# Kernel tuning notes

Measured on AMD Instinct MI355X. Metric: run time of the kernel, lower is better.

Reference implementation:

```python
import jax, jax.numpy as jnp
import numpy as np


def setup_inputs() -> dict:
    key = jax.random.key(0)
    ks = jax.random.split(key, 5)
    B, C, H, W = 8, 256, 64, 64
    Cr = 32  # in_channels // reduction_ratio
    s_in = 1.0 / np.sqrt(C)
    x = jax.random.normal(ks[0], (B, C, H, W), dtype=jnp.float32)
    Wq = jax.random.normal(ks[1], (Cr, C), dtype=jnp.float32) * s_in
    Wk = jax.random.normal(ks[2], (Cr, C), dtype=jnp.float32) * s_in
    Wv = jax.random.normal(ks[3], (C, C), dtype=jnp.float32) * s_in
    bq = jnp.zeros((Cr,), dtype=jnp.float32)
    bk = jnp.zeros((Cr,), dtype=jnp.float32)
    bv = jnp.zeros((C,), dtype=jnp.float32)
    gamma = jnp.ones((1,), dtype=jnp.float32)
    return {"x": x, "Wq": Wq, "bq": bq, "Wk": Wk, "bk": bk, "Wv": Wv, "bv": bv, "gamma": gamma}


def reference(x, Wq, bq, Wk, bk, Wv, bv, gamma):
    B, C, H, W = x.shape
    N = H * W
    xf = x.reshape(B, C, N)  # 1x1 conv == per-pixel linear over channels
    q = jnp.einsum('oc,bcn->bon', Wq, xf) + bq[None, :, None]   # [B, Cr, N]
    k = jnp.einsum('oc,bcn->bon', Wk, xf) + bk[None, :, None]   # [B, Cr, N]
    v = jnp.einsum('oc,bcn->bon', Wv, xf) + bv[None, :, None]   # [B, C, N]
    # correlations[b, i, j] = sum_c q[b, c, i] * k[b, c, j]
    corr = jnp.einsum('bci,bcj->bij', q, k)                     # [B, N, N]
    # NOTE: softmax over dim=1 (the i / query axis), as in the original torch code
    beta = jax.nn.softmax(corr, axis=1)
    att = gamma[0] * jnp.einsum('bci,bij->bcj', v, beta)        # [B, C, N]
    return att.reshape(B, C, H, W) + x
```

## Files before the change

### kernel.cpp

```cpp
#include <hip/hip_runtime.h>
#include <hip/hip_bf16.h>

typedef short bf16x8 __attribute__((ext_vector_type(8)));
typedef float f32x4 __attribute__((ext_vector_type(4)));
typedef unsigned short u16;

#define LOG2E 1.44269504088896340736f
#define AS1 __attribute__((address_space(1)))
#define AS3 __attribute__((address_space(3)))

__device__ __forceinline__ u16 f2bf(float f) {
    unsigned u = __float_as_uint(f);
    u += 0x7fffu + ((u >> 16) & 1u);
    return (u16)(u >> 16);
}
__device__ __forceinline__ float bf2f(u16 h) {
    return __uint_as_float(((unsigned)h) << 16);
}
__device__ __forceinline__ void gload_lds16(const void* g, void* l) {
    __builtin_amdgcn_global_load_lds((const AS1 unsigned int*)g,
                                     (AS3 unsigned int*)l, 16, 0, 0);
}

__global__ void k_prep(const float* __restrict__ Wq, const float* __restrict__ bq,
                       const float* __restrict__ Wk, const float* __restrict__ bk,
                       const float* __restrict__ Wv, const float* __restrict__ bv,
                       u16* __restrict__ Whi, u16* __restrict__ Wlo,
                       float* __restrict__ bias) {
    int idx = blockIdx.x * 256 + threadIdx.x;
    if (idx >= 320 * 256) return;
    int row = idx >> 8, c = idx & 255;
    float w, b;
    if (row < 256)      { w = Wv[row * 256 + c];                  b = bv[row]; }
    else if (row < 288) { w = Wq[(row - 256) * 256 + c] * LOG2E;  b = bq[row - 256] * LOG2E; }
    else                { w = Wk[(row - 288) * 256 + c];          b = bk[row - 288]; }
    u16 hi = f2bf(w);
    Whi[idx] = hi;
    Wlo[idx] = f2bf(w - bf2f(hi));
    if (c == 0) bias[row] = b;
}

#define XPAD 264

__global__ __launch_bounds__(256) void k_proj(
    const float* __restrict__ x, const u16* __restrict__ Whi,
    const u16* __restrict__ Wlo, const float* __restrict__ bias,
    u16* __restrict__ qt, u16* __restrict__ kt, u16* __restrict__ vbf) {
    __shared__ __attribute__((aligned(16))) u16 xh[64 * XPAD];
    __shared__ __attribute__((aligned(16))) u16 xl[64 * XPAD];
    int bid = blockIdx.x;
    int b = bid & 7, nt = bid >> 3;
    int n0 = nt * 64;
    int t = threadIdx.x;
    int lane = t & 63, w = t >> 6;
    int lr = lane & 15, lk = lane >> 4;

    {
        int n = t & 63;
        int cg = t >> 6;
        for (int it = 0; it < 8; ++it) {
            int c8 = (it * 4 + cg) * 8;
            bf16x8 hv, lv;
#pragma unroll
            for (int u = 0; u < 8; ++u) {
                float xv = x[((size_t)(b * 256 + c8 + u)) * 4096 + n0 + n];
                u16 hu = f2bf(xv);
                hv[u] = (short)hu;
                lv[u] = (short)f2bf(xv - bf2f(hu));
            }
            *(bf16x8*)&xh[n * XPAD + c8] = hv;
            *(bf16x8*)&xl[n * XPAD + c8] = lv;
        }
    }
    __syncthreads();

    f32x4 acc[5][4];
#pragma unroll
    for (int i = 0; i < 5; i++)
#pragma unroll
        for (int j = 0; j < 4; j++) acc[i][j] = (f32x4){0.f, 0.f, 0.f, 0.f};

    for (int cs = 0; cs < 8; ++cs) {
        int c0 = cs * 32;
        bf16x8 ah[5], al[5], bh[4], bl[4];
#pragma unroll
        for (int mt = 0; mt < 5; ++mt) {
            int row = (w * 5 + mt) * 16 + lr;
            ah[mt] = *(const bf16x8*)&Whi[row * 256 + c0 + lk * 8];
            al[mt] = *(const bf16x8*)&Wlo[row * 256 + c0 + lk * 8];
        }
#pragma unroll
        for (int ns = 0; ns < 4; ++ns) {
            int np = ns * 16 + lr;
            bh[ns] = *(const bf16x8*)&xh[np * XPAD + c0 + lk * 8];
            bl[ns] = *(const bf16x8*)&xl[np * XPAD + c0 + lk * 8];
        }
#pragma unroll
        for (int mt = 0; mt < 5; ++mt)
#pragma unroll
            for (int ns = 0; ns < 4; ++ns) {
                acc[mt][ns] = __builtin_amdgcn_mfma_f32_16x16x32_bf16(ah[mt], bh[ns], acc[mt][ns], 0, 0, 0);
                acc[mt][ns] = __builtin_amdgcn_mfma_f32_16x16x32_bf16(ah[mt], bl[ns], acc[mt][ns], 0, 0, 0);
                acc[mt][ns] = __builtin_amdgcn_mfma_f32_16x16x32_bf16(al[mt], bh[ns], acc[mt][ns], 0, 0, 0);
            }
    }

#pragma unroll
    for (int mt = 0; mt < 5; ++mt) {
        int tile = w * 5 + mt;
#pragma unroll
        for (int ns = 0; ns < 4; ++ns) {
#pragma unroll
            for (int r = 0; r < 4; ++r) {
                int row = tile * 16 + lk * 4 + r;
                int n = n0 + ns * 16 + lr;
                float val = acc[mt][ns][r] + bias[row];
                if (row < 256) {
                    vbf[((size_t)(b * 256 + row)) * 4096 + n] = f2bf(val);
                } else if (row < 288) {
                    u16 hi = f2bf(val);
                    size_t base = ((size_t)(b * 4096 + n)) * 64 + (row - 256);
                    qt[base] = hi;
                    qt[base + 32] = f2bf(val - bf2f(hi));
                } else {
                    u16 hi = f2bf(val);
                    size_t base = ((size_t)(b * 4096 + n)) * 64 + (row - 288);
                    kt[base] = hi;
                    kt[base + 32] = f2bf(val - bf2f(hi));
                }
            }
        }
    }
}

__global__ __launch_bounds__(256) void k_bound(
    const u16* __restrict__ qt, const u16* __restrict__ kt,
    float* __restrict__ Sh) {
    __shared__ float rq[4], rk[4];
    int b = blockIdx.x;
    int t = threadIdx.x;
    int lane = t & 63, w = t >> 6;
    float qm = 0.f, km = 0.f;
    for (int n = t; n < 4096; n += 256) {
        size_t base = ((size_t)(b * 4096 + n)) * 64;
        float sq = 0.f, sk = 0.f;
#pragma unroll
        for (int g = 0; g < 4; ++g) {
            bf16x8 vq = *(const bf16x8*)&qt[base + g * 8];
            bf16x8 vk = *(const bf16x8*)&kt[base + g * 8];
#pragma unroll
            for (int u = 0; u < 8; ++u) {
                float a = bf2f((u16)vq[u]), c = bf2f((u16)vk[u]);
                sq += a * a;
                sk += c * c;
            }
        }
        qm = fmaxf(qm, sq);
        km = fmaxf(km, sk);
    }
#pragma unroll
    for (int d = 1; d < 64; d <<= 1) {
        qm = fmaxf(qm, __shfl_xor(qm, d));
        km = fmaxf(km, __shfl_xor(km, d));
    }
    if (lane == 0) { rq[w] = qm; rk[w] = km; }
    __syncthreads();
    if (t == 0) {
        float a = fmaxf(fmaxf(rq[0], rq[1]), fmaxf(rq[2], rq[3]));
        float c = fmaxf(fmaxf(rk[0], rk[1]), fmaxf(rk[2], rk[3]));
        Sh[b] = fmaxf(0.f, sqrtf(a) * sqrtf(c) - 80.f);
    }
}

#define PSTR 40

__global__ __launch_bounds__(256) void k_attn(
    const u16* __restrict__ qt, const u16* __restrict__ kt,
    const u16* __restrict__ vbf, const float* __restrict__ Sh,
    const float* __restrict__ x, const float* __restrict__ gamma,
    float* __restrict__ out) {
    __shared__ __attribute__((aligned(16))) u16 qlds[2][32 * 64];
    __shared__ __attribute__((aligned(16))) u16 vlds[2][256 * 32];
    __shared__ __attribute__((aligned(16))) u16 P[2][4][16][PSTR];
    __shared__ float Ls[4][16];
    int bid = blockIdx.x;
    int b = bid & 7, jt = bid >> 3;
    int t = threadIdx.x;
    int lane = t & 63, w = t >> 6;
    int lr = lane & 15, lk = lane >> 4;
    int j0 = jt * 64;

    size_t kb = ((size_t)(b * 4096 + j0 + w * 16 + lr)) * 64 + lk * 8;
    bf16x8 khi = *(const bf16x8*)&kt[kb];
    bf16x8 klo = *(const bf16x8*)&kt[kb + 32];
    float shift = Sh[b];

    auto stage = [&](int nb, int i0) {
#pragma unroll
        for (int n = 0; n < 4; ++n) {
            int I = w * 4 + n;
            int c = I * 16 + (lane >> 2);
            int s = (lane & 3) ^ ((lane >> 3) & 3);
            gload_lds16(vbf + ((size_t)(b * 256 + c)) * 4096 + i0 + s * 8,
                        &vlds[nb][I * 512]);
        }
        {
            int i = w * 8 + (lane >> 3);
            int s = (lane & 7) ^ ((lane >> 3) & 7);
            gload_lds16(qt + ((size_t)(b * 4096 + i0 + i)) * 64 + s * 8,
                        &qlds[nb][w * 512]);
        }
    };

    f32x4 acc[4][4];
#pragma unroll
    for (int i = 0; i < 4; i++)
#pragma unroll
        for (int j = 0; j < 4; j++) acc[i][j] = (f32x4){0.f, 0.f, 0.f, 0.f};
    float lsum = 0.f;
    const f32x4 zero = {0.f, 0.f, 0.f, 0.f};

    stage(0, 0);
    __syncthreads();

    for (int it = 0; it < 128; ++it) {
        int buf = it & 1;
        stage(buf ^ 1, ((it + 1) & 127) * 32);

        bf16x8 qh[2], ql[2];
#pragma unroll
        for (int g = 0; g < 2; ++g) {
            int i = g * 16 + lr;
            int ph = lk ^ (lr & 7);
            qh[g] = *(const bf16x8*)&qlds[buf][i * 64 + ph * 8];
            ql[g] = *(const bf16x8*)&qlds[buf][i * 64 + (ph ^ 4) * 8];
        }
        f32x4 s[2];
#pragma unroll
        for (int g = 0; g < 2; ++g) {
            s[g] = __builtin_amdgcn_mfma_f32_16x16x32_bf16(qh[g], khi, zero, 0, 0, 0);
            s[g] = __builtin_amdgcn_mfma_f32_16x16x32_bf16(qh[g], klo, s[g], 0, 0, 0);
            s[g] = __builtin_amdgcn_mfma_f32_16x16x32_bf16(ql[g], khi, s[g], 0, 0, 0);
        }

#pragma unroll
        for (int g = 0; g < 2; ++g) {
            float p0 = exp2f(s[g][0] - shift), p1 = exp2f(s[g][1] - shift);
            float p2 = exp2f(s[g][2] - shift), p3 = exp2f(s[g][3] - shift);
            lsum += (p0 + p1) + (p2 + p3);
            uint2 pk;
            pk.x = ((unsigned)f2bf(p1) << 16) | f2bf(p0);
            pk.y = ((unsigned)f2bf(p3) << 16) | f2bf(p2);
            *(uint2*)&P[buf][w][lr][g * 16 + lk * 4] = pk;
        }

        bf16x8 av[4];
#pragma unroll
        for (int ct = 0; ct < 4; ++ct) {
            int c = w * 64 + ct * 16 + lr;
            int ph = lk ^ ((lr >> 1) & 3);
            av[ct] = *(const bf16x8*)&vlds[buf][c * 32 + ph * 8];
        }

        __syncthreads();

        bf16x8 bp[4];
#pragma unroll
        for (int js = 0; js < 4; ++js)
            bp[js] = *(const bf16x8*)&P[buf][js][lr][lk * 8];
#pragma unroll
        for (int ct = 0; ct < 4; ++ct)
#pragma unroll
            for (int js = 0; js < 4; ++js)
                acc[ct][js] = __builtin_amdgcn_mfma_f32_16x16x32_bf16(av[ct], bp[js], acc[ct][js], 0, 0, 0);
    }

    lsum += __shfl_xor(lsum, 16);
    lsum += __shfl_xor(lsum, 32);
    if (lane < 16) Ls[w][lr] = lsum;
    __syncthreads();
    float g = gamma[0];
    float linv[4];
#pragma unroll
    for (int js = 0; js < 4; ++js) linv[js] = g / Ls[js][lr];
#pragma unroll
    for (int ct = 0; ct < 4; ++ct)
#pragma unroll
        for (int r = 0; r < 4; ++r) {
            int c = w * 64 + ct * 16 + lk * 4 + r;
            size_t base = ((size_t)(b * 256 + c)) * 4096 + j0;
#pragma unroll
            for (int js = 0; js < 4; ++js) {
                int j = js * 16 + lr;
                out[base + j] = acc[ct][js][r] * linv[js] + x[base + j];
            }
        }
}

extern "C" void kernel_launch(void* const* d_in, const int* in_sizes, int n_in,
                              void* d_out, int out_size, void* d_ws, size_t ws_size,
                              hipStream_t stream) {
    const float* x = (const float*)d_in[0];
    const float* Wq = (const float*)d_in[1];
    const float* bq = (const float*)d_in[2];
    const float* Wk = (const float*)d_in[3];
    const float* bk = (const float*)d_in[4];
    const float* Wv = (const float*)d_in[5];
    const float* bv = (const float*)d_in[6];
    const float* gamma = (const float*)d_in[7];

    char* ws = (char*)d_ws;
    u16* Whi = (u16*)ws;
    u16* Wlo = (u16*)(ws + 163840);
    float* bias = (float*)(ws + 327680);
    u16* qt = (u16*)(ws + 329216);
    u16* kt = (u16*)(ws + 329216 + 4194304);
    u16* vbf = (u16*)(ws + 329216 + 8388608);
    float* Shf = (float*)(ws + 329216 + 25165824);

    k_prep<<<320, 256, 0, stream>>>(Wq, bq, Wk, bk, Wv, bv, Whi, Wlo, bias);
    k_proj<<<512, 256, 0, stream>>>(x, Whi, Wlo, bias, qt, kt, vbf);
    k_bound<<<8, 256, 0, stream>>>(qt, kt, Shf);
    k_attn<<<512, 256, 0, stream>>>(qt, kt, vbf, Shf, x, gamma, (float*)d_out);
}
```

Before: 300.8 us.

## Split attention output channels across two blocks to double grid size

Splits the 256 output channels of the attention kernel into two halves handled by separate blocks, doubling the grid from 512 to 1024 blocks and halving the V staging buffer and accumulator registers per block. This is meant to raise occupancy and fill all CUs (512 blocks over 256 CUs gives only two waves of work). The exchange is that QK^T scores and the exp/softmax numerator are recomputed twice per (batch, column tile). Global address computation is also hoisted out of the staging lambda.

```diff
diff --git a/kernel.cpp b/kernel.cpp
--- a/kernel.cpp
+++ b/kernel.cpp
@@ -180,41 +180,39 @@
     const float* __restrict__ x, const float* __restrict__ gamma,
     float* __restrict__ out) {
     __shared__ __attribute__((aligned(16))) u16 qlds[2][32 * 64];
-    __shared__ __attribute__((aligned(16))) u16 vlds[2][256 * 32];
+    __shared__ __attribute__((aligned(16))) u16 vlds[2][128 * 32];
     __shared__ __attribute__((aligned(16))) u16 P[2][4][16][PSTR];
     __shared__ float Ls[4][16];
     int bid = blockIdx.x;
-    int b = bid & 7, jt = bid >> 3;
+    int b = bid & 7;
+    int rest = bid >> 3;
+    int jt = rest & 63, ch = rest >> 6;
     int t = threadIdx.x;
     int lane = t & 63, w = t >> 6;
     int lr = lane & 15, lk = lane >> 4;
     int j0 = jt * 64;
+    int c0 = ch * 128;
 
     size_t kb = ((size_t)(b * 4096 + j0 + w * 16 + lr)) * 64 + lk * 8;
     bf16x8 khi = *(const bf16x8*)&kt[kb];
     bf16x8 klo = *(const bf16x8*)&kt[kb + 32];
     float shift = Sh[b];
 
+    const int vs = (lane & 3) ^ ((lane >> 3) & 3);
+    const u16* vsrc0 = vbf + ((size_t)(b * 256 + c0 + (w * 2 + 0) * 16 + (lane >> 2))) * 4096 + vs * 8;
+    const u16* vsrc1 = vbf + ((size_t)(b * 256 + c0 + (w * 2 + 1) * 16 + (lane >> 2))) * 4096 + vs * 8;
+    const u16* qsrc = qt + ((size_t)(b * 4096 + w * 8 + (lane >> 3))) * 64
+                         + (((lane & 7) ^ ((lane >> 3) & 7))) * 8;
+
     auto stage = [&](int nb, int i0) {
-#pragma unroll
-        for (int n = 0; n < 4; ++n) {
-            int I = w * 4 + n;
-            int c = I * 16 + (lane >> 2);
-            int s = (lane & 3) ^ ((lane >> 3) & 3);
-            gload_lds16(vbf + ((size_t)(b * 256 + c)) * 4096 + i0 + s * 8,
-                        &vlds[nb][I * 512]);
-        }
-        {
-            int i = w * 8 + (lane >> 3);
-            int s = (lane & 7) ^ ((lane >> 3) & 7);
-            gload_lds16(qt + ((size_t)(b * 4096 + i0 + i)) * 64 + s * 8,
-                        &qlds[nb][w * 512]);
-        }
+        gload_lds16(vsrc0 + i0, &vlds[nb][(w * 2 + 0) * 512]);
+        gload_lds16(vsrc1 + i0, &vlds[nb][(w * 2 + 1) * 512]);
+        gload_lds16(qsrc + (size_t)i0 * 64, &qlds[nb][w * 512]);
     };
 
-    f32x4 acc[4][4];
-#pragma unroll
-    for (int i = 0; i < 4; i++)
+    f32x4 acc[2][4];
+#pragma unroll
+    for (int i = 0; i < 2; i++)
 #pragma unroll
         for (int j = 0; j < 4; j++) acc[i][j] = (f32x4){0.f, 0.f, 0.f, 0.f};
     float lsum = 0.f;
@@ -254,12 +252,12 @@
             *(uint2*)&P[buf][w][lr][g * 16 + lk * 4] = pk;
         }
 
-        bf16x8 av[4];
-#pragma unroll
-        for (int ct = 0; ct < 4; ++ct) {
-            int c = w * 64 + ct * 16 + lr;
+        bf16x8 av[2];
+#pragma unroll
+        for (int ct = 0; ct < 2; ++ct) {
+            int cl = w * 32 + ct * 16 + lr;
             int ph = lk ^ ((lr >> 1) & 3);
-            av[ct] = *(const bf16x8*)&vlds[buf][c * 32 + ph * 8];
+            av[ct] = *(const bf16x8*)&vlds[buf][cl * 32 + ph * 8];
         }
 
         __syncthreads();
@@ -269,7 +267,7 @@
         for (int js = 0; js < 4; ++js)
             bp[js] = *(const bf16x8*)&P[buf][js][lr][lk * 8];
 #pragma unroll
-        for (int ct = 0; ct < 4; ++ct)
+        for (int ct = 0; ct < 2; ++ct)
 #pragma unroll
             for (int js = 0; js < 4; ++js)
                 acc[ct][js] = __builtin_amdgcn_mfma_f32_16x16x32_bf16(av[ct], bp[js], acc[ct][js], 0, 0, 0);
@@ -284,10 +282,10 @@
 #pragma unroll
     for (int js = 0; js < 4; ++js) linv[js] = g / Ls[js][lr];
 #pragma unroll
-    for (int ct = 0; ct < 4; ++ct)
+    for (int ct = 0; ct < 2; ++ct)
 #pragma unroll
         for (int r = 0; r < 4; ++r) {
-            int c = w * 64 + ct * 16 + lk * 4 + r;
+            int c = c0 + w * 32 + ct * 16 + lk * 4 + r;
             size_t base = ((size_t)(b * 256 + c)) * 4096 + j0;
 #pragma unroll
             for (int js = 0; js < 4; ++js) {
@@ -321,5 +319,5 @@
     k_prep<<<320, 256, 0, stream>>>(Wq, bq, Wk, bk, Wv, bv, Whi, Wlo, bias);
     k_proj<<<512, 256, 0, stream>>>(x, Whi, Wlo, bias, qt, kt, vbf);
     k_bound<<<8, 256, 0, stream>>>(qt, kt, Shf);
-    k_attn<<<512, 256, 0, stream>>>(qt, kt, vbf, Shf, x, gamma, (float*)d_out);
-}
+    k_attn<<<1024, 256, 0, stream>>>(qt, kt, vbf, Shf, x, gamma, (float*)d_out);
+}
```

New measurement: 384.7 us. 1.28x slower.
